# Performance work log

Hardware: AMD Instinct MI355X
Metric: run time of the kernel (lower is better)

## Reference

```python
import jax, jax.numpy as jnp
import numpy as np

B = 16384      # batch
F = 26         # onehot fields
E = 32         # embedding_dim
L = 50         # multihot bag length
V = 1000000    # num_embeddings
CT = 13        # continuous features
D0, D1, D2, D3 = 909, 512, 256, 1
LEAKY = 0.01


def _leaky(x):
    return jnp.where(x >= 0, x, LEAKY * x)


def setup_inputs() -> dict:
    key = jax.random.key(0)
    ks = jax.random.split(key, 16)
    inp = {
        "onehot_i": jax.random.randint(ks[0], (B, F), 0, V),
        "onehot_x": jax.random.uniform(ks[1], (B, F), dtype=jnp.float32),
        "multihot_i1": jax.random.randint(ks[2], (B, L), 0, V),
        "multihot_x1": jax.random.uniform(ks[3], (B, L), dtype=jnp.float32),
        "multihot_i2": jax.random.randint(ks[4], (B, L), 0, V),
        "multihot_x2": jax.random.uniform(ks[5], (B, L), dtype=jnp.float32),
        "ctns": jax.random.normal(ks[6], (B, CT), dtype=jnp.float32),
        # learned parameters
        "wide_table": jax.random.normal(ks[7], (V, 1), dtype=jnp.float32) * 0.02,
        "deep_table": jax.random.normal(ks[8], (V, E), dtype=jnp.float32) * 0.02,
        "w2": jax.random.normal(ks[9], (D1, D0), dtype=jnp.float32) * (1.0 / np.sqrt(D0)),
        "b2": jnp.zeros((D1,), dtype=jnp.float32),
        "w3": jax.random.normal(ks[10], (D2, D1), dtype=jnp.float32) * (1.0 / np.sqrt(D1)),
        "b3": jnp.zeros((D2,), dtype=jnp.float32),
        "w4": jax.random.normal(ks[11], (D3, D2), dtype=jnp.float32) * (1.0 / np.sqrt(D2)),
        "b4": jnp.zeros((D3,), dtype=jnp.float32),
    }
    return inp


def reference(onehot_i, onehot_x, multihot_i1, multihot_x1, multihot_i2,
              multihot_x2, ctns, wide_table, deep_table, w2, b2, w3, b3, w4, b4):
    # ---- wide part ----
    # Original broadcasts the [B,F,1] wide embedding against x repeated E times,
    # then sums over all columns. That equals E * sum_f(w[idx]*x).
    wide_sum = (wide_table[onehot_i, 0] * onehot_x).sum(axis=1)          # [B]
    wide_sum = wide_sum + (wide_table[multihot_i1, 0] * multihot_x1).sum(axis=1)
    wide_sum = wide_sum + (wide_table[multihot_i2, 0] * multihot_x2).sum(axis=1)
    wide_out = E * wide_sum                                              # [B]

    # ---- deep part: gather, scale by field weight, pool multihot bags ----
    d_one = (deep_table[onehot_i] * onehot_x[:, :, None]).reshape(B, F * E)   # [B, F*E]
    d_m1 = (deep_table[multihot_i1] * multihot_x1[:, :, None]).sum(axis=1)    # [B, E]
    d_m2 = (deep_table[multihot_i2] * multihot_x2[:, :, None]).sum(axis=1)    # [B, E]
    x = jnp.concatenate([d_one, d_m1, d_m2, ctns], axis=1)                    # [B, D0]

    # dropout p=0.0 (deterministic reference)
    x = _leaky(x @ w2.T + b2)
    x = _leaky(x @ w3.T + b3)
    x = (x @ w4.T + b4).squeeze(-1)                                           # [B]
    return jax.nn.sigmoid(x + wide_out)
```

## Files before the change

### kernel.cpp

```cpp
#include <hip/hip_runtime.h>
#include <hip/hip_bf16.h>
#include <math.h>

#define B_   16384
#define F_   26
#define E_   32
#define L_   50
#define CT_  13
#define D0_  909
#define D0P  928
#define D1_  512
#define D2_  256

typedef __bf16 bf16x8 __attribute__((ext_vector_type(8)));
typedef float f32x4 __attribute__((ext_vector_type(4)));

__device__ inline float bf2f(unsigned short u) {
    union { unsigned int i; float f; } v; v.i = ((unsigned int)u) << 16; return v.f;
}

__device__ inline void gld_lds16(const void* g, void* l) {
    __builtin_amdgcn_global_load_lds(
        (const __attribute__((address_space(1))) unsigned int*)g,
        (__attribute__((address_space(3))) unsigned int*)l, 16, 0, 0);
}

__global__ __launch_bounds__(256) void cvt_pad_w2(const float* __restrict__ w,
                                                  __hip_bfloat16* __restrict__ o) {
    int i = blockIdx.x * 256 + threadIdx.x;
    int r = i / D0P, c = i - r * D0P;
    float v = (c < D0_) ? w[r * D0_ + c] : 0.f;
    o[i] = __float2bfloat16(v);
}

__global__ __launch_bounds__(256) void cvt_w3(const float* __restrict__ w,
                                              __hip_bfloat16* __restrict__ o) {
    int i = blockIdx.x * 256 + threadIdx.x;
    o[i] = __float2bfloat16(w[i]);
}

__global__ __launch_bounds__(256) void embed_kernel(
    const int* __restrict__ oi, const float* __restrict__ ox,
    const int* __restrict__ i1, const float* __restrict__ x1,
    const int* __restrict__ i2, const float* __restrict__ x2,
    const float* __restrict__ ct, const float* __restrict__ wtab,
    const float* __restrict__ dtab,
    __hip_bfloat16* __restrict__ x0, float* __restrict__ wide)
{
    const int s    = blockIdx.x * 4 + (threadIdx.x >> 6);
    const int lane = threadIdx.x & 63;
    const int half = lane >> 5;
    const int e    = lane & 31;
    __hip_bfloat16* xrow = x0 + (size_t)s * D0P;

    for (int f = half; f < F_; f += 2) {
        int idx  = oi[s * F_ + f];
        float xv = ox[s * F_ + f];
        float v  = dtab[(size_t)idx * E_ + e] * xv;
        xrow[f * E_ + e] = __float2bfloat16(v);
    }
    float a1 = 0.f, a2 = 0.f;
    for (int j = half; j < L_; j += 2) {
        a1 += dtab[(size_t)i1[s * L_ + j] * E_ + e] * x1[s * L_ + j];
        a2 += dtab[(size_t)i2[s * L_ + j] * E_ + e] * x2[s * L_ + j];
    }
    a1 += __shfl_xor(a1, 32);
    a2 += __shfl_xor(a2, 32);
    if (half == 0) xrow[F_ * E_ + e]      = __float2bfloat16(a1);
    else           xrow[F_ * E_ + E_ + e] = __float2bfloat16(a2);
    if (half == 0) {
        float v = (e < CT_) ? ct[s * CT_ + e] : 0.f;
        xrow[F_ * E_ + 2 * E_ + e] = __float2bfloat16(v);
    }
    float acc = 0.f;
    for (int t = lane; t < F_ + 2 * L_; t += 64) {
        int idx; float xv;
        if (t < F_)            { idx = oi[s * F_ + t];            xv = ox[s * F_ + t]; }
        else if (t < F_ + L_)  { int j = t - F_;       idx = i1[s * L_ + j]; xv = x1[s * L_ + j]; }
        else                   { int j = t - F_ - L_;  idx = i2[s * L_ + j]; xv = x2[s * L_ + j]; }
        acc += wtab[idx] * xv;
    }
    for (int o = 32; o; o >>= 1) acc += __shfl_xor(acc, o);
    if (lane == 0) wide[s] = (float)E_ * acc;
}

template<int N, int K, bool ACT>
__global__ __launch_bounds__(256) void gemm_bias(
    const __hip_bfloat16* __restrict__ A,
    const __hip_bfloat16* __restrict__ W,
    const float* __restrict__ bias,
    __hip_bfloat16* __restrict__ C, int MBLKS)
{
    __shared__ __hip_bfloat16 As[128 * 32];
    __shared__ __hip_bfloat16 Bs[128 * 32];

    const int bm   = blockIdx.x % MBLKS;
    const int bn   = blockIdx.x / MBLKS;
    const int tid  = threadIdx.x;
    const int lane = tid & 63;
    const int w    = tid >> 6;
    const int wm   = w >> 1, wn = w & 1;

    f32x4 acc[4][4] = {};

    const int srow = lane >> 2;
    const int scol = (lane & 3) * 8;
    const __hip_bfloat16* Aw0 = A + ((size_t)bm * 128 + w * 32 + srow) * K + scol;
    const __hip_bfloat16* Aw1 = Aw0 + (size_t)16 * K;
    const __hip_bfloat16* Ww0 = W + ((size_t)bn * 128 + w * 32 + srow) * K + scol;
    const __hip_bfloat16* Ww1 = Ww0 + (size_t)16 * K;
    char* AsW = (char*)As + w * 2048;
    char* BsW = (char*)Bs + w * 2048;

    const int fr = lane & 15;
    const int kg = (lane >> 4) * 8;

    for (int k0 = 0; k0 < K; k0 += 32) {
        gld_lds16(Aw0 + k0, AsW);
        gld_lds16(Aw1 + k0, AsW + 1024);
        gld_lds16(Ww0 + k0, BsW);
        gld_lds16(Ww1 + k0, BsW + 1024);
        __syncthreads();

        bf16x8 af[4], bfv[4];
#pragma unroll
        for (int i = 0; i < 4; i++)
            af[i] = *(const bf16x8*)(As + (wm * 64 + i * 16 + fr) * 32 + kg);
#pragma unroll
        for (int i = 0; i < 4; i++)
            bfv[i] = *(const bf16x8*)(Bs + (wn * 64 + i * 16 + fr) * 32 + kg);
#pragma unroll
        for (int i = 0; i < 4; i++)
#pragma unroll
            for (int j = 0; j < 4; j++)
                acc[i][j] = __builtin_amdgcn_mfma_f32_16x16x32_bf16(af[i], bfv[j], acc[i][j], 0, 0, 0);
        __syncthreads();
    }

    float bv[4];
#pragma unroll
    for (int j = 0; j < 4; j++) bv[j] = bias[bn * 128 + wn * 64 + j * 16 + fr];
    const int crow0 = bm * 128 + wm * 64 + (lane >> 4) * 4;
    const int ccol0 = bn * 128 + wn * 64 + fr;
#pragma unroll
    for (int i = 0; i < 4; i++)
#pragma unroll
        for (int j = 0; j < 4; j++)
#pragma unroll
            for (int r = 0; r < 4; r++) {
                float v = acc[i][j][r] + bv[j];
                if (ACT) v = (v >= 0.f) ? v : 0.01f * v;
                C[(size_t)(crow0 + i * 16 + r) * N + ccol0 + j * 16] = __float2bfloat16(v);
            }
}

__global__ __launch_bounds__(256) void final_kernel(
    const __hip_bfloat16* __restrict__ h2, const float* __restrict__ w4,
    const float* __restrict__ b4, const float* __restrict__ wide,
    float* __restrict__ out)
{
    const int s    = blockIdx.x * 4 + (threadIdx.x >> 6);
    const int lane = threadIdx.x & 63;
    const unsigned short* hp = (const unsigned short*)(h2 + (size_t)s * D2_);
    ushort4 hv = *(const ushort4*)(hp + lane * 4);
    float4  wv = *(const float4*)(w4 + lane * 4);
    float acc = bf2f(hv.x) * wv.x + bf2f(hv.y) * wv.y + bf2f(hv.z) * wv.z + bf2f(hv.w) * wv.w;
    for (int o = 32; o; o >>= 1) acc += __shfl_xor(acc, o);
    if (lane == 0) {
        float x = acc + b4[0] + wide[s];
        out[s] = 1.f / (1.f + expf(-x));
    }
}

extern "C" void kernel_launch(void* const* d_in, const int* in_sizes, int n_in,
                              void* d_out, int out_size, void* d_ws, size_t ws_size,
                              hipStream_t stream) {
    const int*   oi  = (const int*)  d_in[0];
    const float* ox  = (const float*)d_in[1];
    const int*   i1  = (const int*)  d_in[2];
    const float* x1  = (const float*)d_in[3];
    const int*   i2  = (const int*)  d_in[4];
    const float* x2  = (const float*)d_in[5];
    const float* ct  = (const float*)d_in[6];
    const float* wt  = (const float*)d_in[7];
    const float* dt  = (const float*)d_in[8];
    const float* w2  = (const float*)d_in[9];
    const float* b2  = (const float*)d_in[10];
    const float* w3  = (const float*)d_in[11];
    const float* b3  = (const float*)d_in[12];
    const float* w4  = (const float*)d_in[13];
    const float* b4  = (const float*)d_in[14];
    float* out = (float*)d_out;

    char* ws = (char*)d_ws;
    __hip_bfloat16* x0b = (__hip_bfloat16*)(ws);
    __hip_bfloat16* h1b = (__hip_bfloat16*)(ws + 30408704);
    __hip_bfloat16* h2b = (__hip_bfloat16*)(ws + 47185920);
    float*          wid = (float*)         (ws + 55574528);
    __hip_bfloat16* w2b = (__hip_bfloat16*)(ws + 55640064);
    __hip_bfloat16* w3b = (__hip_bfloat16*)(ws + 56590336);

    cvt_pad_w2<<<1856, 256, 0, stream>>>(w2, w2b);
    cvt_w3   <<<512,  256, 0, stream>>>(w3, w3b);
    embed_kernel<<<4096, 256, 0, stream>>>(oi, ox, i1, x1, i2, x2, ct, wt, dt, x0b, wid);
    gemm_bias<D1_, D0P, true ><<<128 * (D1_ / 128), 256, 0, stream>>>(x0b, w2b, b2, h1b, 128);
    gemm_bias<D2_, D1_, true ><<<128 * (D2_ / 128), 256, 0, stream>>>(h1b, w3b, b3, h2b, 128);
    final_kernel<<<4096, 256, 0, stream>>>(h2b, w4, b4, wid, out);
}
```

Measured before the change: 131.0 us.

## Vectorize embedding gathers with float4 per lane and merge weight conversion kernels

The embed kernel now has each lane fetch a float4 of an embedding row, with 8 lanes covering one 32-wide row, so one wavefront handles 8 rows at a time instead of 2. Loops are fully unrolled so more independent gathers are in flight, and bag partial sums are reduced with xor shuffles across the 8-lane groups. The two weight conversion kernels are merged into one launch to save launch overhead. The cost is more shuffle work and higher register pressure.

```diff
diff --git a/kernel.cpp b/kernel.cpp
--- a/kernel.cpp
+++ b/kernel.cpp
@@ -18,6 +18,11 @@
 __device__ inline float bf2f(unsigned short u) {
     union { unsigned int i; float f; } v; v.i = ((unsigned int)u) << 16; return v.f;
 }
+__device__ inline unsigned short f2b(float f) {
+    union { __hip_bfloat16 h; unsigned short u; } v;
+    v.h = __float2bfloat16(f);
+    return v.u;
+}
 
 __device__ inline void gld_lds16(const void* g, void* l) {
     __builtin_amdgcn_global_load_lds(
@@ -25,18 +30,21 @@
         (__attribute__((address_space(3))) unsigned int*)l, 16, 0, 0);
 }
 
-__global__ __launch_bounds__(256) void cvt_pad_w2(const float* __restrict__ w,
-                                                  __hip_bfloat16* __restrict__ o) {
+#define W2N (D1_ * D0P)
+#define W3N (D2_ * D1_)
+__global__ __launch_bounds__(256) void cvt_weights(
+    const float* __restrict__ w2, const float* __restrict__ w3,
+    __hip_bfloat16* __restrict__ o2, __hip_bfloat16* __restrict__ o3)
+{
     int i = blockIdx.x * 256 + threadIdx.x;
-    int r = i / D0P, c = i - r * D0P;
-    float v = (c < D0_) ? w[r * D0_ + c] : 0.f;
-    o[i] = __float2bfloat16(v);
-}
-
-__global__ __launch_bounds__(256) void cvt_w3(const float* __restrict__ w,
-                                              __hip_bfloat16* __restrict__ o) {
-    int i = blockIdx.x * 256 + threadIdx.x;
-    o[i] = __float2bfloat16(w[i]);
+    if (i < W2N) {
+        int r = i / D0P, c = i - r * D0P;
+        float v = (c < D0_) ? w2[r * D0_ + c] : 0.f;
+        o2[i] = __float2bfloat16(v);
+    } else {
+        int j = i - W2N;
+        if (j < W3N) o3[j] = __float2bfloat16(w3[j]);
+    }
 }
 
 __global__ __launch_bounds__(256) void embed_kernel(
@@ -49,30 +57,63 @@
 {
     const int s    = blockIdx.x * 4 + (threadIdx.x >> 6);
     const int lane = threadIdx.x & 63;
-    const int half = lane >> 5;
-    const int e    = lane & 31;
+    const int g    = lane >> 3;
+    const int l    = lane & 7;
     __hip_bfloat16* xrow = x0 + (size_t)s * D0P;
-
-    for (int f = half; f < F_; f += 2) {
-        int idx  = oi[s * F_ + f];
-        float xv = ox[s * F_ + f];
-        float v  = dtab[(size_t)idx * E_ + e] * xv;
-        xrow[f * E_ + e] = __float2bfloat16(v);
-    }
-    float a1 = 0.f, a2 = 0.f;
-    for (int j = half; j < L_; j += 2) {
-        a1 += dtab[(size_t)i1[s * L_ + j] * E_ + e] * x1[s * L_ + j];
-        a2 += dtab[(size_t)i2[s * L_ + j] * E_ + e] * x2[s * L_ + j];
-    }
-    a1 += __shfl_xor(a1, 32);
-    a2 += __shfl_xor(a2, 32);
-    if (half == 0) xrow[F_ * E_ + e]      = __float2bfloat16(a1);
-    else           xrow[F_ * E_ + E_ + e] = __float2bfloat16(a2);
-    if (half == 0) {
-        float v = (e < CT_) ? ct[s * CT_ + e] : 0.f;
-        xrow[F_ * E_ + 2 * E_ + e] = __float2bfloat16(v);
+    const float4* dt4 = (const float4*)dtab;
+
+#pragma unroll
+    for (int f0 = 0; f0 < 32; f0 += 8) {
+        int f = f0 + g;
+        if (f < F_) {
+            int   idx = oi[s * F_ + f];
+            float xv  = ox[s * F_ + f];
+            float4 v  = dt4[(size_t)idx * 8 + l];
+            ushort4 o;
+            o.x = f2b(v.x * xv); o.y = f2b(v.y * xv);
+            o.z = f2b(v.z * xv); o.w = f2b(v.w * xv);
+            *(ushort4*)(xrow + f * E_ + l * 4) = o;
+        }
+    }
+
+    float4 a1 = {0.f, 0.f, 0.f, 0.f}, a2 = {0.f, 0.f, 0.f, 0.f};
+#pragma unroll
+    for (int j0 = 0; j0 < 56; j0 += 8) {
+        int j = j0 + g;
+        if (j < L_) {
+            int   k1 = i1[s * L_ + j];  float xv1 = x1[s * L_ + j];
+            int   k2 = i2[s * L_ + j];  float xv2 = x2[s * L_ + j];
+            float4 v1 = dt4[(size_t)k1 * 8 + l];
+            float4 v2 = dt4[(size_t)k2 * 8 + l];
+            a1.x = fmaf(v1.x, xv1, a1.x); a1.y = fmaf(v1.y, xv1, a1.y);
+            a1.z = fmaf(v1.z, xv1, a1.z); a1.w = fmaf(v1.w, xv1, a1.w);
+            a2.x = fmaf(v2.x, xv2, a2.x); a2.y = fmaf(v2.y, xv2, a2.y);
+            a2.z = fmaf(v2.z, xv2, a2.z); a2.w = fmaf(v2.w, xv2, a2.w);
+        }
+    }
+#pragma unroll
+    for (int m = 8; m < 64; m <<= 1) {
+        a1.x += __shfl_xor(a1.x, m); a1.y += __shfl_xor(a1.y, m);
+        a1.z += __shfl_xor(a1.z, m); a1.w += __shfl_xor(a1.w, m);
+        a2.x += __shfl_xor(a2.x, m); a2.y += __shfl_xor(a2.y, m);
+        a2.z += __shfl_xor(a2.z, m); a2.w += __shfl_xor(a2.w, m);
+    }
+    if (g == 0) {
+        ushort4 o;
+        o.x = f2b(a1.x); o.y = f2b(a1.y); o.z = f2b(a1.z); o.w = f2b(a1.w);
+        *(ushort4*)(xrow + F_ * E_ + l * 4) = o;
+    }
+    if (g == 1) {
+        ushort4 o;
+        o.x = f2b(a2.x); o.y = f2b(a2.y); o.z = f2b(a2.z); o.w = f2b(a2.w);
+        *(ushort4*)(xrow + F_ * E_ + E_ + l * 4) = o;
+    }
+    if (lane < E_) {
+        float v = (lane < CT_) ? ct[s * CT_ + lane] : 0.f;
+        xrow[F_ * E_ + 2 * E_ + lane] = __float2bfloat16(v);
     }
     float acc = 0.f;
+#pragma unroll
     for (int t = lane; t < F_ + 2 * L_; t += 64) {
         int idx; float xv;
         if (t < F_)            { idx = oi[s * F_ + t];            xv = ox[s * F_ + t]; }
@@ -200,8 +241,7 @@
     __hip_bfloat16* w2b = (__hip_bfloat16*)(ws + 55640064);
     __hip_bfloat16* w3b = (__hip_bfloat16*)(ws + 56590336);
 
-    cvt_pad_w2<<<1856, 256, 0, stream>>>(w2, w2b);
-    cvt_w3   <<<512,  256, 0, stream>>>(w3, w3b);
+    cvt_weights<<<(W2N + W3N + 255) / 256, 256, 0, stream>>>(w2, w3, w2b, w3b);
     embed_kernel<<<4096, 256, 0, stream>>>(oi, ox, i1, x1, i2, x2, ct, wt, dt, x0b, wid);
     gemm_bias<D1_, D0P, true ><<<128 * (D1_ / 128), 256, 0, stream>>>(x0b, w2b, b2, h1b, 128);
     gemm_bias<D2_, D1_, true ><<<128 * (D2_ / 128), 256, 0, stream>>>(h1b, w3b, b3, h2b, 128);
```

Measured after the change: 126.5 us. 1.04x faster.
